# Optimization experiments

Measured on AMD Instinct MI355X. Metric: run time of the kernel, lower is better.

The kernel has to match this reference:

```python
import jax, jax.numpy as jnp
import numpy as np

N_NODES = 50000
N_EDGES = 800000
IN_DIM = 128
EMB = 128
EDGE_DIM = 16
N_LAYERS = 4
BATCH = 64


def setup_inputs() -> dict:
    key = jax.random.key(0)
    ks = jax.random.split(key, 12)
    x = jax.random.normal(ks[0], (N_NODES, IN_DIM), dtype=jnp.float32)
    edge_index = jax.random.randint(ks[1], (2, N_EDGES), 0, N_NODES, dtype=jnp.int64)
    edge_attr = jax.random.normal(ks[2], (N_EDGES, EDGE_DIM), dtype=jnp.float32)
    batch = jnp.sort(jax.random.randint(ks[3], (N_NODES,), 0, BATCH, dtype=jnp.int64))

    def glorot(k, shape):
        fan_in = shape[-2]
        return jax.random.normal(k, shape, dtype=jnp.float32) / jnp.sqrt(jnp.float32(fan_in))

    msg_in = 2 * EMB + EDGE_DIM  # [h_src, h_dst, edge_attr]
    upd_in = 2 * EMB             # [h, aggregated_messages]
    return {
        "x": x,
        "edge_index": edge_index,
        "edge_attr": edge_attr,
        "batch": batch,
        "W_in": glorot(ks[4], (IN_DIM, EMB)),
        "b_in": jnp.zeros((EMB,), jnp.float32),
        "W_msg": glorot(ks[5], (N_LAYERS, msg_in, EMB)),
        "b_msg": jnp.zeros((N_LAYERS, EMB), jnp.float32),
        "W_upd": glorot(ks[6], (N_LAYERS, upd_in, EMB)),
        "b_upd": jnp.zeros((N_LAYERS, EMB), jnp.float32),
        "W_pred": glorot(ks[7], (EMB, 1)),
        "b_pred": jnp.zeros((1,), jnp.float32),
    }


def reference(x, edge_index, edge_attr, batch,
              W_in, b_in, W_msg, b_msg, W_upd, b_upd, W_pred, b_pred):
    n_nodes = x.shape[0]
    src, dst = edge_index[0], edge_index[1]

    # lin_in
    h = x @ W_in + b_in  # [N, EMB]

    # stacked message-passing layers with residual adds
    for l in range(W_msg.shape[0]):  # small fixed layer loop
        # per-edge message: relu(Linear([h_src, h_dst, e]))
        m_in = jnp.concatenate([h[src], h[dst], edge_attr], axis=-1)  # [E, 2*EMB+ED]
        m = jax.nn.relu(m_in @ W_msg[l] + b_msg[l])                    # [E, EMB]
        # sum-aggregate messages at destination nodes
        agg = jax.ops.segment_sum(m, dst, num_segments=n_nodes)       # [N, EMB]
        # node update: relu(Linear([h, agg])); residual add (h = h + conv(h))
        u_in = jnp.concatenate([h, agg], axis=-1)                      # [N, 2*EMB]
        h = h + jax.nn.relu(u_in @ W_upd[l] + b_upd[l])

    # global mean pool over graphs in the batch
    counts = jax.ops.segment_sum(jnp.ones((n_nodes,), h.dtype), batch, num_segments=BATCH)
    h_graph = jax.ops.segment_sum(h, batch, num_segments=BATCH) / jnp.maximum(counts, 1.0)[:, None]

    # lin_pred + view(-1)
    out = h_graph @ W_pred + b_pred  # [BATCH, 1]
    return out.reshape(-1)
```

## Files before the change

### kernel.cpp

```cpp
#include <hip/hip_runtime.h>


#define THREADS 256

typedef __attribute__((ext_vector_type(8))) short short8v;
typedef __attribute__((ext_vector_type(4))) float f32x4;

__device__ inline unsigned short f2bf(float f)
{
    unsigned int u = __float_as_uint(f);
    return (unsigned short)((u + 0x7FFFu + ((u >> 16) & 1u)) >> 16);
}

__global__ __launch_bounds__(THREADS)
void wconv_all(const float* __restrict__ W_in, const float* __restrict__ W_msg,
               const float* __restrict__ W_upd, unsigned short* __restrict__ wbf)
{
    int b = blockIdx.x;
    int job, kb;
    if (b < 576) { job = b >> 6; kb = b & 63; }
    else         { int r = b - 576; job = 9 + (r >> 7); kb = r & 127; }

    const float* src;
    unsigned short* dst;
    int K;
    if (job == 0)      { src = W_in;                                  dst = wbf;                       K = 128; }
    else if (job <= 4) { int l = job - 1; src = W_msg + (size_t)l * 272 * 128;             dst = wbf + 16384  + l * 16384; K = 128; }
    else if (job <= 8) { int l = job - 5; src = W_msg + (size_t)l * 272 * 128 + 128 * 128; dst = wbf + 81920  + l * 16384; K = 128; }
    else               { int l = job - 9; src = W_upd + (size_t)l * 256 * 128;             dst = wbf + 147456 + l * 32768; K = 256; }

    int i = kb * 256 + threadIdx.x;
    int k = i >> 7, n = i & 127;
    dst[n * K + k] = f2bf(src[i]);
}

template<bool RELU, bool RESID>
__global__ __launch_bounds__(THREADS)
void gemm_bf16(const float* __restrict__ X1, const float* __restrict__ X2,
               const unsigned short* __restrict__ Wt, const float* __restrict__ bias,
               const float* __restrict__ resid, float* __restrict__ C,
               int M, int K)
{
    __shared__ unsigned short Als[64 * 40];
    __shared__ unsigned short Bls[128 * 40];

    const int t = threadIdx.x;
    const int w = t >> 6;
    const int l = t & 63;
    const int r  = l & 15;
    const int kb = l >> 4;
    const int mBase = blockIdx.x * 64;

    f32x4 acc[8];
#pragma unroll
    for (int c = 0; c < 8; c++) acc[c] = (f32x4){0.f, 0.f, 0.f, 0.f};

    const int am = t >> 2;
    const int ak = (t & 3) * 8;
    const int agr = min(mBase + am, M - 1);

    for (int k0 = 0; k0 < K; k0 += 32) {
        const float* Xs = X1;
        int ko = k0;
        if (k0 >= 128) { Xs = X2; ko = k0 - 128; }

        float4 f0 = *reinterpret_cast<const float4*>(Xs + (size_t)agr * 128 + ko + ak);
        float4 f1 = *reinterpret_cast<const float4*>(Xs + (size_t)agr * 128 + ko + ak + 4);
        const int c0 = t, c1 = t + 256;
        const int bn0 = c0 >> 2, bk0 = (c0 & 3) * 8;
        const int bn1 = c1 >> 2, bk1 = (c1 & 3) * 8;
        short8v wv0 = *reinterpret_cast<const short8v*>(Wt + (size_t)bn0 * K + k0 + bk0);
        short8v wv1 = *reinterpret_cast<const short8v*>(Wt + (size_t)bn1 * K + k0 + bk1);

        __syncthreads();

        unsigned short* ap = &Als[am * 40 + ak];
        ap[0] = f2bf(f0.x); ap[1] = f2bf(f0.y); ap[2] = f2bf(f0.z); ap[3] = f2bf(f0.w);
        ap[4] = f2bf(f1.x); ap[5] = f2bf(f1.y); ap[6] = f2bf(f1.z); ap[7] = f2bf(f1.w);
        *reinterpret_cast<short8v*>(&Bls[bn0 * 40 + bk0]) = wv0;
        *reinterpret_cast<short8v*>(&Bls[bn1 * 40 + bk1]) = wv1;

        __syncthreads();

        const short8v a = *reinterpret_cast<const short8v*>(&Als[(w * 16 + r) * 40 + kb * 8]);
#pragma unroll
        for (int c = 0; c < 8; c++) {
            const short8v b = *reinterpret_cast<const short8v*>(&Bls[(c * 16 + r) * 40 + kb * 8]);
            acc[c] = __builtin_amdgcn_mfma_f32_16x16x32_bf16(a, b, acc[c], 0, 0, 0);
        }
    }

    const int col  = r;
    const int rbase = mBase + w * 16 + kb * 4;
#pragma unroll
    for (int c = 0; c < 8; c++) {
        const int gc = c * 16 + col;
        float bv = bias ? bias[gc] : 0.f;
#pragma unroll
        for (int j = 0; j < 4; j++) {
            int gr = rbase + j;
            if (gr >= M) continue;
            float v = acc[c][j] + bv;
            if (RELU)  v = fmaxf(v, 0.f);
            if (RESID) v += resid[(size_t)gr * 128 + gc];
            C[(size_t)gr * 128 + gc] = v;
        }
    }
}

__global__ __launch_bounds__(THREADS)
void zero_i32(int* __restrict__ p, int n)
{
    int i = blockIdx.x * blockDim.x + threadIdx.x;
    int stride = gridDim.x * blockDim.x;
    for (; i < n; i += stride) p[i] = 0;
}


__global__ __launch_bounds__(THREADS)
void csr_hist(const int* __restrict__ edst, int* __restrict__ deg, int nE)
{
    int i = blockIdx.x * blockDim.x + threadIdx.x;
    int stride = gridDim.x * blockDim.x;
    for (; i < nE; i += stride) atomicAdd(&deg[edst[i]], 1);
}

__global__ __launch_bounds__(THREADS)
void scan_stage1(const int* __restrict__ deg, int* __restrict__ incl,
                 int* __restrict__ psum, int n)
{
    __shared__ int buf[THREADS];
    const int t = threadIdx.x;
    const int base = blockIdx.x * 1024 + t * 4;

    int v0 = (base + 0 < n) ? deg[base + 0] : 0;
    int v1 = (base + 1 < n) ? deg[base + 1] : 0;
    int v2 = (base + 2 < n) ? deg[base + 2] : 0;
    int v3 = (base + 3 < n) ? deg[base + 3] : 0;
    const int s = v0 + v1 + v2 + v3;

    buf[t] = s;
    __syncthreads();
#pragma unroll
    for (int off = 1; off < THREADS; off <<= 1) {
        int x = (t >= off) ? buf[t - off] : 0;
        __syncthreads();
        buf[t] += x;
        __syncthreads();
    }
    const int excl = buf[t] - s;

    if (base + 0 < n) incl[base + 0] = excl + v0;
    if (base + 1 < n) incl[base + 1] = excl + v0 + v1;
    if (base + 2 < n) incl[base + 2] = excl + v0 + v1 + v2;
    if (base + 3 < n) incl[base + 3] = excl + s;
    if (t == THREADS - 1) psum[blockIdx.x] = buf[THREADS - 1];
}

__global__ __launch_bounds__(THREADS)
void scan_stage2(int* __restrict__ psum, int nb)
{
    __shared__ int buf[THREADS];
    const int t = threadIdx.x;
    int v = (t < nb) ? psum[t] : 0;
    buf[t] = v;
    __syncthreads();
#pragma unroll
    for (int off = 1; off < THREADS; off <<= 1) {
        int x = (t >= off) ? buf[t - off] : 0;
        __syncthreads();
        buf[t] += x;
        __syncthreads();
    }
    if (t < nb) psum[t] = buf[t] - v;
}

__global__ __launch_bounds__(THREADS)
void scan_stage3(const int* __restrict__ incl, const int* __restrict__ deg,
                 const int* __restrict__ psum, int* __restrict__ rowptr,
                 int* __restrict__ wp, int n, int nE)
{
    int i = blockIdx.x * blockDim.x + threadIdx.x;
    int stride = gridDim.x * blockDim.x;
    for (; i < n; i += stride) {
        int ex = incl[i] - deg[i] + psum[i >> 10];
        rowptr[i] = ex;
        wp[i]     = ex;
    }
    if (blockIdx.x == 0 && threadIdx.x == 0) rowptr[n] = nE;
}

__global__ __launch_bounds__(THREADS)
void csr_scatter(const int* __restrict__ esrc, const int* __restrict__ edst,
                 const float* __restrict__ eattr, int* __restrict__ wp,
                 int* __restrict__ col, float* __restrict__ eattrp, int nE)
{
    int i = blockIdx.x * blockDim.x + threadIdx.x;
    int stride = gridDim.x * blockDim.x;
    for (; i < nE; i += stride) {
        int d = edst[i];
        int pos = atomicAdd(&wp[d], 1);
        col[pos] = esrc[i];
        const float4* src4 = reinterpret_cast<const float4*>(eattr + (size_t)i * 16);
        float4*       dst4 = reinterpret_cast<float4*>(eattrp + (size_t)pos * 16);
        dst4[0] = src4[0]; dst4[1] = src4[1]; dst4[2] = src4[2]; dst4[3] = src4[3];
    }
}

__global__ __launch_bounds__(THREADS)
void edge_agg(const float* __restrict__ A, const float* __restrict__ Bb,
              const float* __restrict__ eattrp, const int* __restrict__ col,
              const int* __restrict__ rowptr, const float* __restrict__ Wm3,
              float* __restrict__ agg, int nN)
{
    __shared__ float W3s[16 * 128];
    const int t = threadIdx.x;

    *reinterpret_cast<float4*>(&W3s[t * 4])        = *reinterpret_cast<const float4*>(Wm3 + t * 4);
    *reinterpret_cast<float4*>(&W3s[1024 + t * 4]) = *reinterpret_cast<const float4*>(Wm3 + 1024 + t * 4);
    __syncthreads();

    const int lane = t & 63;
    const int wid  = __builtin_amdgcn_readfirstlane(t >> 6);
    const int d    = blockIdx.x * 4 + wid;
    if (d >= nN) return;

    float2 w[16];
#pragma unroll
    for (int k = 0; k < 16; k++)
        w[k] = *reinterpret_cast<const float2*>(&W3s[k * 128 + lane * 2]);

    const float2 b2 = *reinterpret_cast<const float2*>(Bb + (size_t)d * 128 + lane * 2);
    float2 acc = make_float2(0.f, 0.f);

    const int beg = rowptr[d], end = rowptr[d + 1];
    for (int e = beg; e < end; e++) {
        const int s = col[e];
        const float2 a2 = *reinterpret_cast<const float2*>(A + (size_t)s * 128 + lane * 2);
        float vx = a2.x + b2.x;
        float vy = a2.y + b2.y;
        const float4* ea4 = reinterpret_cast<const float4*>(eattrp + (size_t)e * 16);
        const float4 e0 = ea4[0], e1 = ea4[1], e2 = ea4[2], e3 = ea4[3];
        const float ek[16] = {e0.x, e0.y, e0.z, e0.w, e1.x, e1.y, e1.z, e1.w,
                              e2.x, e2.y, e2.z, e2.w, e3.x, e3.y, e3.z, e3.w};
#pragma unroll
        for (int k = 0; k < 16; k++) {
            vx = fmaf(ek[k], w[k].x, vx);
            vy = fmaf(ek[k], w[k].y, vy);
        }
        acc.x += fmaxf(vx, 0.f);
        acc.y += fmaxf(vy, 0.f);
    }
    *reinterpret_cast<float2*>(agg + (size_t)d * 128 + lane * 2) = acc;
}


__global__ __launch_bounds__(THREADS)
void pool_partial(const float* __restrict__ h, const int* __restrict__ batch,
                  float* __restrict__ hgsum, int n)
{
    const int t    = threadIdx.x;
    const int c    = t & 127;
    const int half = t >> 7;
    const int beg  = blockIdx.x * 256;
    const int end  = min(beg + 256, n);
    if (beg >= n) return;

    int   cur = -1;
    float acc = 0.f;
    for (int r = beg + half; r < end; r += 2) {
        int g = batch[r];
        if (g != cur) {
            if (cur >= 0) atomicAdd(&hgsum[(size_t)cur * 128 + c], acc);
            cur = g; acc = 0.f;
        }
        acc += h[(size_t)r * 128 + c];
    }
    if (cur >= 0) atomicAdd(&hgsum[(size_t)cur * 128 + c], acc);
}

__global__ __launch_bounds__(THREADS)
void pool_final(const float* __restrict__ hgsum, const int* __restrict__ batch,
                const float* __restrict__ Wp, const float* __restrict__ bp,
                float* __restrict__ out, int n)
{
    __shared__ float red[128];
    const int g = blockIdx.x;
    const int t = threadIdx.x;
    if (t >= 128) return;

    int lo, hi;
    {
        int a = 0, b = n;
        while (a < b) { int m = (a + b) >> 1; if (batch[m] < g) a = m + 1; else b = m; }
        lo = a;
        b = n;
        while (a < b) { int m = (a + b) >> 1; if (batch[m] < g + 1) a = m + 1; else b = m; }
        hi = a;
    }
    const int cnt = hi - lo;

    float v = hgsum[(size_t)g * 128 + t] / (float)max(cnt, 1);
    red[t] = v * Wp[t];
    __syncthreads();
    for (int off = 64; off > 0; off >>= 1) {
        if (t < off) red[t] += red[t + off];
        __syncthreads();
    }
    if (t == 0) out[g] = red[0] + bp[0];
}

extern "C" void kernel_launch(void* const* d_in, const int* in_sizes, int n_in,
                              void* d_out, int out_size, void* d_ws, size_t ws_size,
                              hipStream_t stream)
{
    const float* x      = (const float*)d_in[0];
    const int*   ei     = (const int*)  d_in[1];
    const float* eattr  = (const float*)d_in[2];
    const int*   batch  = (const int*)  d_in[3];
    const float* W_in   = (const float*)d_in[4];
    const float* b_in   = (const float*)d_in[5];
    const float* W_msg  = (const float*)d_in[6];
    const float* b_msg  = (const float*)d_in[7];
    const float* W_upd  = (const float*)d_in[8];
    const float* b_upd  = (const float*)d_in[9];
    const float* W_pred = (const float*)d_in[10];
    const float* b_pred = (const float*)d_in[11];
    float* out = (float*)d_out;

    const int nN = in_sizes[0] / 128;
    const int nE = in_sizes[1] / 2;
    const int* esrc = ei;
    const int* edst = ei + nE;

    float* h      = (float*)d_ws;
    float* A      = h      + (size_t)nN * 128;
    float* Bb     = A      + (size_t)nN * 128;
    float* agg    = Bb     + (size_t)nN * 128;
    float* eattrp = agg    + (size_t)nN * 128;
    float* hgsum  = eattrp + (size_t)nE * 16;
    int*   rowptr = (int*)(hgsum + 64 * 128);
    int*   wp     = rowptr + (nN + 1);
    int*   deg    = wp     + nN;
    int*   incl   = deg    + nN;
    int*   psum   = incl   + nN;
    int*   col    = psum   + 256;
    size_t wboff = ((size_t)(col + nE) - (size_t)d_ws + 63) & ~(size_t)63;
    unsigned short* wbf = (unsigned short*)((char*)d_ws + wboff);
    unsigned short* wt_in  = wbf;
    unsigned short* wt_m1  = wbf + 16384;
    unsigned short* wt_m2  = wbf + 81920;
    unsigned short* wt_up  = wbf + 147456;

    dim3 blk(THREADS);
    const int gx = (nN + 63) / 64;
    const int nChunks = (nN + 1023) / 1024;

    wconv_all<<<1088, blk, 0, stream>>>(W_in, W_msg, W_upd, wbf);

    zero_i32<<<64, blk, 0, stream>>>(deg, nN);
    csr_hist<<<256, blk, 0, stream>>>(edst, deg, nE);
    scan_stage1<<<nChunks, blk, 0, stream>>>(deg, incl, psum, nN);
    scan_stage2<<<1, blk, 0, stream>>>(psum, nChunks);
    scan_stage3<<<64, blk, 0, stream>>>(incl, deg, psum, rowptr, wp, nN, nE);
    csr_scatter<<<256, blk, 0, stream>>>(esrc, edst, eattr, wp, col, eattrp, nE);

    gemm_bf16<false, false><<<gx, blk, 0, stream>>>(x, nullptr, wt_in, b_in, nullptr, h, nN, 128);

    for (int l = 0; l < 4; l++) {
        const float* Wm3 = W_msg + (size_t)l * 272 * 128 + 256 * 128;
        const float* bm  = b_msg + l * 128;
        const float* bu  = b_upd + l * 128;

        gemm_bf16<false, false><<<gx, blk, 0, stream>>>(h, nullptr, wt_m1 + l * 16384, nullptr, nullptr, A,  nN, 128);
        gemm_bf16<false, false><<<gx, blk, 0, stream>>>(h, nullptr, wt_m2 + l * 16384, bm,      nullptr, Bb, nN, 128);

        edge_agg<<<(nN + 3) / 4, blk, 0, stream>>>(A, Bb, eattrp, col, rowptr, Wm3, agg, nN);

        gemm_bf16<true, true><<<gx, blk, 0, stream>>>(h, agg, wt_up + l * 32768, bu, h, h, nN, 256);
    }

    zero_i32<<<16, blk, 0, stream>>>((int*)hgsum, 64 * 128);
    pool_partial<<<(nN + 255) / 256, blk, 0, stream>>>(h, batch, hgsum, nN);
    pool_final<<<64, blk, 0, stream>>>(hgsum, batch, W_pred, b_pred, out, nN);
}
```

Before: 666.1 us.

## Store intermediate activations in bf16 to halve gather and GEMM input traffic

GEMM inputs and outputs for h, A, Bb and agg are now stored as bf16 instead of fp32, with x converted once by a new kernel. The GEMMs load bf16 tiles directly instead of converting on the fly, and edge_agg gathers 4-byte bf16 pairs per lane rather than float2. An fp32 copy of h is kept for the residual and pooling. This targets memory bandwidth, mainly the random per-edge gather of A rows, at the cost of extra rounding in A, Bb and agg.

Result: no change. 666.7 us (+0.1%).

```diff
diff --git a/kernel.cpp b/kernel.cpp
--- a/kernel.cpp
+++ b/kernel.cpp
@@ -34,12 +34,25 @@
     dst[n * K + k] = f2bf(src[i]);
 }
 
-template<bool RELU, bool RESID>
-__global__ __launch_bounds__(THREADS)
-void gemm_bf16(const float* __restrict__ X1, const float* __restrict__ X2,
+__global__ __launch_bounds__(THREADS)
+void f32_to_bf16(const float* __restrict__ in, unsigned short* __restrict__ out, int n4)
+{
+    int i = blockIdx.x * blockDim.x + threadIdx.x;
+    int stride = gridDim.x * blockDim.x;
+    for (; i < n4; i += stride) {
+        float4 v = reinterpret_cast<const float4*>(in)[i];
+        unsigned int lo = f2bf(v.x) | ((unsigned int)f2bf(v.y) << 16);
+        unsigned int hi = f2bf(v.z) | ((unsigned int)f2bf(v.w) << 16);
+        reinterpret_cast<uint2*>(out)[i] = make_uint2(lo, hi);
+    }
+}
+
+template<bool RELU, bool RESID, bool WF32>
+__global__ __launch_bounds__(THREADS)
+void gemm_bf16(const unsigned short* __restrict__ X1, const unsigned short* __restrict__ X2,
                const unsigned short* __restrict__ Wt, const float* __restrict__ bias,
-               const float* __restrict__ resid, float* __restrict__ C,
-               int M, int K)
+               const float* __restrict__ resid, float* __restrict__ Cf,
+               unsigned short* __restrict__ Cbf, int M, int K)
 {
     __shared__ unsigned short Als[64 * 40];
     __shared__ unsigned short Bls[128 * 40];
@@ -59,24 +72,22 @@
     const int ak = (t & 3) * 8;
     const int agr = min(mBase + am, M - 1);
 
+    const int c0 = t, c1 = t + 256;
+    const int bn0 = c0 >> 2, bk0 = (c0 & 3) * 8;
+    const int bn1 = c1 >> 2, bk1 = (c1 & 3) * 8;
+
     for (int k0 = 0; k0 < K; k0 += 32) {
-        const float* Xs = X1;
+        const unsigned short* Xs = X1;
         int ko = k0;
         if (k0 >= 128) { Xs = X2; ko = k0 - 128; }
 
-        float4 f0 = *reinterpret_cast<const float4*>(Xs + (size_t)agr * 128 + ko + ak);
-        float4 f1 = *reinterpret_cast<const float4*>(Xs + (size_t)agr * 128 + ko + ak + 4);
-        const int c0 = t, c1 = t + 256;
-        const int bn0 = c0 >> 2, bk0 = (c0 & 3) * 8;
-        const int bn1 = c1 >> 2, bk1 = (c1 & 3) * 8;
+        short8v xv  = *reinterpret_cast<const short8v*>(Xs + (size_t)agr * 128 + ko + ak);
         short8v wv0 = *reinterpret_cast<const short8v*>(Wt + (size_t)bn0 * K + k0 + bk0);
         short8v wv1 = *reinterpret_cast<const short8v*>(Wt + (size_t)bn1 * K + k0 + bk1);
 
         __syncthreads();
 
-        unsigned short* ap = &Als[am * 40 + ak];
-        ap[0] = f2bf(f0.x); ap[1] = f2bf(f0.y); ap[2] = f2bf(f0.z); ap[3] = f2bf(f0.w);
-        ap[4] = f2bf(f1.x); ap[5] = f2bf(f1.y); ap[6] = f2bf(f1.z); ap[7] = f2bf(f1.w);
+        *reinterpret_cast<short8v*>(&Als[am * 40 + ak])   = xv;
         *reinterpret_cast<short8v*>(&Bls[bn0 * 40 + bk0]) = wv0;
         *reinterpret_cast<short8v*>(&Bls[bn1 * 40 + bk1]) = wv1;
 
@@ -90,11 +101,10 @@
         }
     }
 
-    const int col  = r;
     const int rbase = mBase + w * 16 + kb * 4;
 #pragma unroll
     for (int c = 0; c < 8; c++) {
-        const int gc = c * 16 + col;
+        const int gc = c * 16 + r;
         float bv = bias ? bias[gc] : 0.f;
 #pragma unroll
         for (int j = 0; j < 4; j++) {
@@ -103,7 +113,8 @@
             float v = acc[c][j] + bv;
             if (RELU)  v = fmaxf(v, 0.f);
             if (RESID) v += resid[(size_t)gr * 128 + gc];
-            C[(size_t)gr * 128 + gc] = v;
+            if (WF32)  Cf[(size_t)gr * 128 + gc] = v;
+            Cbf[(size_t)gr * 128 + gc] = f2bf(v);
         }
     }
 }
@@ -208,10 +219,10 @@
 }
 
 __global__ __launch_bounds__(THREADS)
-void edge_agg(const float* __restrict__ A, const float* __restrict__ Bb,
+void edge_agg(const unsigned short* __restrict__ A, const unsigned short* __restrict__ Bb,
               const float* __restrict__ eattrp, const int* __restrict__ col,
               const int* __restrict__ rowptr, const float* __restrict__ Wm3,
-              float* __restrict__ agg, int nN)
+              unsigned short* __restrict__ agg, int nN)
 {
     __shared__ float W3s[16 * 128];
     const int t = threadIdx.x;
@@ -230,15 +241,17 @@
     for (int k = 0; k < 16; k++)
         w[k] = *reinterpret_cast<const float2*>(&W3s[k * 128 + lane * 2]);
 
-    const float2 b2 = *reinterpret_cast<const float2*>(Bb + (size_t)d * 128 + lane * 2);
+    const unsigned int bu = *reinterpret_cast<const unsigned int*>(Bb + (size_t)d * 128 + lane * 2);
+    const float b0 = __uint_as_float(bu << 16);
+    const float b1 = __uint_as_float(bu & 0xFFFF0000u);
     float2 acc = make_float2(0.f, 0.f);
 
     const int beg = rowptr[d], end = rowptr[d + 1];
     for (int e = beg; e < end; e++) {
         const int s = col[e];
-        const float2 a2 = *reinterpret_cast<const float2*>(A + (size_t)s * 128 + lane * 2);
-        float vx = a2.x + b2.x;
-        float vy = a2.y + b2.y;
+        const unsigned int au = *reinterpret_cast<const unsigned int*>(A + (size_t)s * 128 + lane * 2);
+        float vx = __uint_as_float(au << 16) + b0;
+        float vy = __uint_as_float(au & 0xFFFF0000u) + b1;
         const float4* ea4 = reinterpret_cast<const float4*>(eattrp + (size_t)e * 16);
         const float4 e0 = ea4[0], e1 = ea4[1], e2 = ea4[2], e3 = ea4[3];
         const float ek[16] = {e0.x, e0.y, e0.z, e0.w, e1.x, e1.y, e1.z, e1.w,
@@ -251,7 +264,8 @@
         acc.x += fmaxf(vx, 0.f);
         acc.y += fmaxf(vy, 0.f);
     }
-    *reinterpret_cast<float2*>(agg + (size_t)d * 128 + lane * 2) = acc;
+    unsigned int o = (unsigned int)f2bf(acc.x) | ((unsigned int)f2bf(acc.y) << 16);
+    *reinterpret_cast<unsigned int*>(agg + (size_t)d * 128 + lane * 2) = o;
 }
 
 
@@ -334,29 +348,31 @@
     const int* edst = ei + nE;
 
     float* h      = (float*)d_ws;
-    float* A      = h      + (size_t)nN * 128;
-    float* Bb     = A      + (size_t)nN * 128;
-    float* agg    = Bb     + (size_t)nN * 128;
-    float* eattrp = agg    + (size_t)nN * 128;
+    float* eattrp = h + (size_t)nN * 128;
     float* hgsum  = eattrp + (size_t)nE * 16;
-    int*   rowptr = (int*)(hgsum + 64 * 128);
+    unsigned short* xbf    = (unsigned short*)(hgsum + 8192);
+    unsigned short* h_bf   = xbf    + (size_t)nN * 128;
+    unsigned short* A_bf   = h_bf   + (size_t)nN * 128;
+    unsigned short* Bb_bf  = A_bf   + (size_t)nN * 128;
+    unsigned short* agg_bf = Bb_bf  + (size_t)nN * 128;
+    unsigned short* wbf    = agg_bf + (size_t)nN * 128;
+    unsigned short* wt_in  = wbf;
+    unsigned short* wt_m1  = wbf + 16384;
+    unsigned short* wt_m2  = wbf + 81920;
+    unsigned short* wt_up  = wbf + 147456;
+    int*   rowptr = (int*)(wbf + 278528);
     int*   wp     = rowptr + (nN + 1);
     int*   deg    = wp     + nN;
     int*   incl   = deg    + nN;
     int*   psum   = incl   + nN;
     int*   col    = psum   + 256;
-    size_t wboff = ((size_t)(col + nE) - (size_t)d_ws + 63) & ~(size_t)63;
-    unsigned short* wbf = (unsigned short*)((char*)d_ws + wboff);
-    unsigned short* wt_in  = wbf;
-    unsigned short* wt_m1  = wbf + 16384;
-    unsigned short* wt_m2  = wbf + 81920;
-    unsigned short* wt_up  = wbf + 147456;
 
     dim3 blk(THREADS);
     const int gx = (nN + 63) / 64;
     const int nChunks = (nN + 1023) / 1024;
 
     wconv_all<<<1088, blk, 0, stream>>>(W_in, W_msg, W_upd, wbf);
+    f32_to_bf16<<<1024, blk, 0, stream>>>(x, xbf, nN * 128 / 4);
 
     zero_i32<<<64, blk, 0, stream>>>(deg, nN);
     csr_hist<<<256, blk, 0, stream>>>(edst, deg, nE);
@@ -365,19 +381,19 @@
     scan_stage3<<<64, blk, 0, stream>>>(incl, deg, psum, rowptr, wp, nN, nE);
     csr_scatter<<<256, blk, 0, stream>>>(esrc, edst, eattr, wp, col, eattrp, nE);
 
-    gemm_bf16<false, false><<<gx, blk, 0, stream>>>(x, nullptr, wt_in, b_in, nullptr, h, nN, 128);
+    gemm_bf16<false, false, true><<<gx, blk, 0, stream>>>(xbf, nullptr, wt_in, b_in, nullptr, h, h_bf, nN, 128);
 
     for (int l = 0; l < 4; l++) {
         const float* Wm3 = W_msg + (size_t)l * 272 * 128 + 256 * 128;
         const float* bm  = b_msg + l * 128;
         const float* bu  = b_upd + l * 128;
 
-        gemm_bf16<false, false><<<gx, blk, 0, stream>>>(h, nullptr, wt_m1 + l * 16384, nullptr, nullptr, A,  nN, 128);
-        gemm_bf16<false, false><<<gx, blk, 0, stream>>>(h, nullptr, wt_m2 + l * 16384, bm,      nullptr, Bb, nN, 128);
-
-        edge_agg<<<(nN + 3) / 4, blk, 0, stream>>>(A, Bb, eattrp, col, rowptr, Wm3, agg, nN);
-
-        gemm_bf16<true, true><<<gx, blk, 0, stream>>>(h, agg, wt_up + l * 32768, bu, h, h, nN, 256);
+        gemm_bf16<false, false, false><<<gx, blk, 0, stream>>>(h_bf, nullptr, wt_m1 + l * 16384, nullptr, nullptr, nullptr, A_bf,  nN, 128);
+        gemm_bf16<false, false, false><<<gx, blk, 0, stream>>>(h_bf, nullptr, wt_m2 + l * 16384, bm,      nullptr, nullptr, Bb_bf, nN, 128);
+
+        edge_agg<<<(nN + 3) / 4, blk, 0, stream>>>(A_bf, Bb_bf, eattrp, col, rowptr, Wm3, agg_bf, nN);
+
+        gemm_bf16<true, true, true><<<gx, blk, 0, stream>>>(h_bf, agg_bf, wt_up + l * 32768, bu, h, h, h_bf, nN, 256);
     }
 
     zero_i32<<<16, blk, 0, stream>>>((int*)hgsum, 64 * 128);
```
